# Performance work log

Measured on AMD Instinct MI355X. Metric: run time of the kernel, lower is better.

The kernel has to match this reference:

```python
import jax, jax.numpy as jnp
import numpy as np

# Model dims
B, T, E, H = 2, 2048, 512, 8
HEAD_DIM = E // H            # 64
NUM_SCALES = 4               # Gauss-Laguerre quadrature nodes
NUM_PRF = 16                 # positive random features per scale
POLY_DIM = 16                # degree-2 TensorSketch dim
EPS = 1e-5
CHUNK = 128                  # chunk size for exact chunked causal linear attention


def setup_inputs() -> dict:
    key = jax.random.key(0)
    ks = jax.random.split(key, 10)
    x = jax.random.normal(ks[0], (B, T, E), jnp.float32)
    sc = 1.0 / np.sqrt(E)  # xavier-ish scale for square projections
    Wq = jax.random.normal(ks[1], (E, E), jnp.float32) * sc
    Wk = jax.random.normal(ks[2], (E, E), jnp.float32) * sc
    Wv = jax.random.normal(ks[3], (E, E), jnp.float32) * sc
    Wo = jax.random.normal(ks[4], (E, E), jnp.float32) * sc
    # FAVOR+ gaussian projections, one block per quadrature scale
    projections = jax.random.normal(ks[5], (NUM_SCALES, NUM_PRF, HEAD_DIM), jnp.float32)
    # Gauss-Laguerre nodes/weights for 1/(C - 2 q.k) = int_0^inf exp(-t(C - 2 q.k)) dt
    nodes, weights = np.polynomial.laguerre.laggauss(NUM_SCALES)
    coef = weights * np.exp(nodes) * np.exp(-nodes * EPS)
    scales = jnp.asarray(np.stack([nodes, coef], axis=1), jnp.float32)  # [S, 2] = (t_s, c_s)
    # degree-2 TensorSketch (count-sketch hashes + rademacher signs)
    sketch_h = jax.random.randint(ks[6], (2, HEAD_DIM), 0, POLY_DIM)
    sketch_s = (jax.random.randint(ks[7], (2, HEAD_DIM), 0, 2) * 2 - 1).astype(jnp.float32)
    return dict(x=x, Wq=Wq, Wk=Wk, Wv=Wv, Wo=Wo, projections=projections,
                scales=scales, sketch_h=sketch_h, sketch_s=sketch_s)


def _features(u, projections, scales, sketch_h, sketch_s):
    """Multi-scale FAVOR+ x TensorSketch feature map for the spherical YAT kernel.

    u: [B,T,H,d], unit-normalized along d. Returns [B,T,H, P*S*m].
    Phi(q).Phi(k) ~= (q.k)^2 / (||q-k||^2 + eps).
    """
    t = scales[:, 0]  # quadrature nodes t_s
    c = scales[:, 1]  # quadrature coeffs w_s e^{t_s} e^{-t_s eps}
    S, m, d = projections.shape
    z = jnp.einsum('smd,bthd->bthsm', projections, u)
    # exp(2 t q.k) via positive RFs; extra e^{-t||u||^2}=e^{-t} (unit sphere) folded in -> -2t
    ef = jnp.exp(jnp.sqrt(2.0 * t)[:, None] * z - 2.0 * t[:, None]) * jnp.sqrt(c / m)[:, None]  # [B,T,H,S,m]
    # degree-2 TensorSketch: countsketch via one-hot matmul, combine with FFT conv
    M1 = sketch_s[0][:, None] * jax.nn.one_hot(sketch_h[0], POLY_DIM, dtype=u.dtype)  # [d,P]
    M2 = sketch_s[1][:, None] * jax.nn.one_hot(sketch_h[1], POLY_DIM, dtype=u.dtype)
    ts = jnp.fft.irfft(jnp.fft.rfft(u @ M1) * jnp.fft.rfft(u @ M2), n=POLY_DIM)  # [B,T,H,P]
    Bs, Ts, Hs = u.shape[:3]
    ef = ef.reshape(Bs, Ts, Hs, S * m)
    return (ts[..., :, None] * ef[..., None, :]).reshape(Bs, Ts, Hs, POLY_DIM * S * m)


def reference(x, Wq, Wk, Wv, Wo, projections, scales, sketch_h, sketch_s):
    Bx, Tx, Ex = x.shape
    d = HEAD_DIM
    q = (x @ Wq).reshape(Bx, Tx, H, d)
    k = (x @ Wk).reshape(Bx, Tx, H, d)
    v = (x @ Wv).reshape(Bx, Tx, H, d)
    # spherical: project q,k to unit sphere
    qn = q / (jnp.linalg.norm(q, axis=-1, keepdims=True) + 1e-6)
    kn = k / (jnp.linalg.norm(k, axis=-1, keepdims=True) + 1e-6)
    fq = _features(qn, projections, scales, sketch_h, sketch_s)  # [B,T,H,F]
    fk = _features(kn, projections, scales, sketch_h, sketch_s)
    F = fq.shape[-1]
    # exact chunked causal linear attention: O(T) state, no [T,T] matrix
    N = Tx // CHUNK
    fq_ = fq.reshape(Bx, N, CHUNK, H, F)
    fk_ = fk.reshape(Bx, N, CHUNK, H, F)
    v_ = v.reshape(Bx, N, CHUNK, H, d)
    kv = jnp.einsum('bnchf,bnchd->bnhfd', fk_, v_)   # per-chunk sum of phi(k) v^T
    kz = fk_.sum(axis=2)                              # [B,N,H,F]
    kv_prev = jnp.concatenate([jnp.zeros_like(kv[:, :1]), jnp.cumsum(kv, axis=1)[:, :-1]], axis=1)
    kz_prev = jnp.concatenate([jnp.zeros_like(kz[:, :1]), jnp.cumsum(kz, axis=1)[:, :-1]], axis=1)
    num = jnp.einsum('bnchf,bnhfd->bnchd', fq_, kv_prev)
    den = jnp.einsum('bnchf,bnhf->bnch', fq_, kz_prev)
    # intra-chunk causal part
    sc = jnp.einsum('bnchf,bnkhf->bnhck', fq_, fk_)
    mask = jnp.tril(jnp.ones((CHUNK, CHUNK), bool))
    scm = jnp.where(mask, sc, 0.0)
    num = num + jnp.einsum('bnhck,bnkhd->bnchd', scm, v_)
    den = den + jnp.swapaxes(scm.sum(axis=-1), 2, 3)
    out = num / (den[..., None] + EPS)
    out = out.reshape(Bx, Tx, Ex) @ Wo
    return out
```

## Files before the change

### kernel.cpp

```cpp
#include <hip/hip_runtime.h>
#include <math.h>

#define B_ 2
#define T_ 2048
#define E_ 512
#define H_ 8
#define D_ 64
#define NCH 16
#define CH 128
#define EPS_ 1e-5f

__global__ __launch_bounds__(256) void gemm512(const float* __restrict__ A,
                                               const float* __restrict__ W,
                                               float* __restrict__ C) {
  __shared__ float As[16][132];
  __shared__ float Bs[16][68];
  const int tid = threadIdx.x;
  const int row0 = blockIdx.x * 128, col0 = blockIdx.y * 64;
  const int ar = tid >> 1, ak = (tid & 1) * 8;
  const int bk = tid >> 4, bc = (tid & 15) * 4;
  const int tx = tid & 15, ty = tid >> 4;
  float4 pa0, pa1, pb;
  pa0 = *(const float4*)(A + (size_t)(row0 + ar) * 512 + ak);
  pa1 = *(const float4*)(A + (size_t)(row0 + ar) * 512 + ak + 4);
  pb  = *(const float4*)(W + (size_t)bk * 512 + col0 + bc);
  float acc[8][4] = {};
  for (int k0 = 0; k0 < 512; k0 += 16) {
    __syncthreads();
    As[ak + 0][ar] = pa0.x; As[ak + 1][ar] = pa0.y; As[ak + 2][ar] = pa0.z; As[ak + 3][ar] = pa0.w;
    As[ak + 4][ar] = pa1.x; As[ak + 5][ar] = pa1.y; As[ak + 6][ar] = pa1.z; As[ak + 7][ar] = pa1.w;
    *(float4*)&Bs[bk][bc] = pb;
    if (k0 < 496) {
      pa0 = *(const float4*)(A + (size_t)(row0 + ar) * 512 + k0 + 16 + ak);
      pa1 = *(const float4*)(A + (size_t)(row0 + ar) * 512 + k0 + 16 + ak + 4);
      pb  = *(const float4*)(W + (size_t)(k0 + 16 + bk) * 512 + col0 + bc);
    }
    __syncthreads();
#pragma unroll
    for (int kk = 0; kk < 16; ++kk) {
      float4 a0 = *(const float4*)&As[kk][ty * 4];
      float4 a1 = *(const float4*)&As[kk][ty * 4 + 64];
      float4 b  = *(const float4*)&Bs[kk][tx * 4];
      float aa[8] = {a0.x, a0.y, a0.z, a0.w, a1.x, a1.y, a1.z, a1.w};
      float bb[4] = {b.x, b.y, b.z, b.w};
#pragma unroll
      for (int i = 0; i < 8; ++i)
#pragma unroll
        for (int j = 0; j < 4; ++j) acc[i][j] += aa[i] * bb[j];
    }
  }
#pragma unroll
  for (int i = 0; i < 8; ++i) {
    const int r = row0 + (i < 4 ? ty * 4 + i : 64 + ty * 4 + (i - 4));
    *(float4*)(C + (size_t)r * 512 + col0 + tx * 4) =
        make_float4(acc[i][0], acc[i][1], acc[i][2], acc[i][3]);
  }
}

__global__ __launch_bounds__(256) void feat_kernel(
    const float* __restrict__ q, const float* __restrict__ k,
    const float* __restrict__ proj, const float* __restrict__ scales,
    const int* __restrict__ sh, const float* __restrict__ ss,
    float* __restrict__ Tq, float* __restrict__ Eq,
    float* __restrict__ Tk, float* __restrict__ Ek) {
  __shared__ float Us[128][68];
  __shared__ float PjT[64][68];
  __shared__ float MT[64][36];
  __shared__ float Ps[128][36];
  __shared__ float csq[64], cmb[64], ccf[64];
  const int tid = threadIdx.x;
  const int isK = blockIdx.y;
  const float* in = (isK ? k : q) + (size_t)blockIdx.x * 8192;
  float* To = isK ? Tk : Tq;
  float* Eo = isK ? Ek : Eq;

#pragma unroll
  for (int j = 0; j < 8; ++j) {
    const int f = tid + 256 * j;
    float4 a = *(const float4*)(in + 4 * f);
    *(float4*)&Us[f >> 4][(f & 15) * 4] = a;
  }
  for (int i = tid; i < 4096; i += 256) PjT[i & 63][i >> 6] = proj[i];
  for (int i = tid; i < 64 * 36; i += 256) (&MT[0][0])[i] = 0.f;
  __syncthreads();

  if (tid < 64) {
    MT[tid][sh[tid]] = ss[tid];
    MT[tid][16 + sh[64 + tid]] = ss[64 + tid];
  } else if (tid < 128) {
    const int c = tid - 64;
    const float t = scales[(c >> 4) * 2], cc = scales[(c >> 4) * 2 + 1];
    csq[c] = sqrtf(2.f * t); cmb[c] = -2.f * t; ccf[c] = sqrtf(cc / 16.f);
  }
  {
    const int r2 = tid >> 1, hf = tid & 1;
    float4 tv[8]; float s2 = 0.f;
#pragma unroll
    for (int j2 = 0; j2 < 8; ++j2) {
      tv[j2] = *(const float4*)&Us[r2][hf * 32 + 4 * j2];
      s2 += tv[j2].x * tv[j2].x + tv[j2].y * tv[j2].y + tv[j2].z * tv[j2].z + tv[j2].w * tv[j2].w;
    }
    s2 += __shfl_xor(s2, 1);
    const float inv = 1.f / (sqrtf(s2) + 1e-6f);
#pragma unroll
    for (int j2 = 0; j2 < 8; ++j2) {
      tv[j2].x *= inv; tv[j2].y *= inv; tv[j2].z *= inv; tv[j2].w *= inv;
      *(float4*)&Us[r2][hf * 32 + 4 * j2] = tv[j2];
    }
  }
  __syncthreads();

  const int tx = tid & 7, ty = tid >> 3;
  const int c0 = tx * 8, pc0 = tx * 4;
  float accz[4][8] = {};
  float accp[4][4] = {};
  for (int d0 = 0; d0 < 64; d0 += 4) {
    float Aar[4][4];
#pragma unroll
    for (int i = 0; i < 4; ++i) {
      float4 a4 = *(const float4*)&Us[ty + 32 * i][d0];
      Aar[i][0] = a4.x; Aar[i][1] = a4.y; Aar[i][2] = a4.z; Aar[i][3] = a4.w;
    }
#pragma unroll
    for (int dd = 0; dd < 4; ++dd) {
      float4 bl = *(const float4*)&PjT[d0 + dd][c0];
      float4 bh = *(const float4*)&PjT[d0 + dd][c0 + 4];
      float4 bm = *(const float4*)&MT[d0 + dd][pc0];
      float bb[8] = {bl.x, bl.y, bl.z, bl.w, bh.x, bh.y, bh.z, bh.w};
      float bp[4] = {bm.x, bm.y, bm.z, bm.w};
#pragma unroll
      for (int i = 0; i < 4; ++i) {
        const float a = Aar[i][dd];
#pragma unroll
        for (int j = 0; j < 8; ++j) accz[i][j] += a * bb[j];
#pragma unroll
        for (int j = 0; j < 4; ++j) accp[i][j] += a * bp[j];
      }
    }
  }

  float sq8[8], mb8[8], cf8[8];
#pragma unroll
  for (int j = 0; j < 8; ++j) { sq8[j] = csq[c0 + j]; mb8[j] = cmb[c0 + j]; cf8[j] = ccf[c0 + j]; }
  const int bx16 = blockIdx.x * 16;
#pragma unroll
  for (int i = 0; i < 4; ++i) {
    const int r = ty + 32 * i;
    const int bt = bx16 + (r >> 3);
    const size_t orow = (size_t)((bt >> 11) * 8 + (r & 7)) * 2048 + (bt & 2047);
    float e[8];
#pragma unroll
    for (int j = 0; j < 8; ++j) e[j] = expf(sq8[j] * accz[i][j] + mb8[j]) * cf8[j];
    *(float4*)(Eo + orow * 64 + c0) = make_float4(e[0], e[1], e[2], e[3]);
    *(float4*)(Eo + orow * 64 + c0 + 4) = make_float4(e[4], e[5], e[6], e[7]);
    *(float4*)&Ps[r][pc0] = make_float4(accp[i][0], accp[i][1], accp[i][2], accp[i][3]);
  }
  __syncthreads();

  const int rr = tid >> 1, hf2 = tid & 1;
  float p1v[16], p2v[16];
#pragma unroll
  for (int j4 = 0; j4 < 4; ++j4) {
    float4 a = *(const float4*)&Ps[rr][j4 * 4];
    p1v[j4 * 4 + 0] = a.x; p1v[j4 * 4 + 1] = a.y; p1v[j4 * 4 + 2] = a.z; p1v[j4 * 4 + 3] = a.w;
    float4 b2 = *(const float4*)&Ps[rr][16 + j4 * 4];
    p2v[j4 * 4 + 0] = b2.x; p2v[j4 * 4 + 1] = b2.y; p2v[j4 * 4 + 2] = b2.z; p2v[j4 * 4 + 3] = b2.w;
  }
  const int bt2 = bx16 + (rr >> 3);
  const size_t orow2 = (size_t)((bt2 >> 11) * 8 + (rr & 7)) * 2048 + (bt2 & 2047);
  float tout[8];
  if (hf2 == 0) {
#pragma unroll
    for (int r8 = 0; r8 < 8; ++r8) {
      float a = 0.f;
#pragma unroll
      for (int j = 0; j < 16; ++j) a += p1v[j] * p2v[(r8 - j) & 15];
      tout[r8] = a;
    }
  } else {
#pragma unroll
    for (int r8 = 0; r8 < 8; ++r8) {
      float a = 0.f;
#pragma unroll
      for (int j = 0; j < 16; ++j) a += p1v[j] * p2v[(8 + r8 - j) & 15];
      tout[r8] = a;
    }
  }
  *(float4*)(To + orow2 * 16 + hf2 * 8) = make_float4(tout[0], tout[1], tout[2], tout[3]);
  *(float4*)(To + orow2 * 16 + hf2 * 8 + 4) = make_float4(tout[4], tout[5], tout[6], tout[7]);
}

__global__ __launch_bounds__(256) void vrelayout(const float* __restrict__ v, float* __restrict__ vh) {
  const int f = blockIdx.x * 256 + threadIdx.x;
  float4 a = *(const float4*)(v + 4 * (size_t)f);
  const int d4 = f & 15, h = (f >> 4) & 7, bt = f >> 7;
  const size_t orow = (size_t)((bt >> 11) * 8 + h) * 2048 + (bt & 2047);
  *(float4*)(vh + orow * 64 + d4 * 4) = a;
}

__global__ __launch_bounds__(256) void kv_kernel(const float* __restrict__ Tk, const float* __restrict__ Ek,
                                                 const float* __restrict__ vh, float* __restrict__ KV) {
  const int bhn = blockIdx.x;
  const int slice = blockIdx.y;
  __shared__ float tks[128][20];
  __shared__ float eks[128][16];
  __shared__ float vs[128][64];
  const int tid = threadIdx.x;
  const size_t rowbase = (size_t)bhn * 128;
  for (int i = tid; i < 2048; i += 256) tks[i >> 4][i & 15] = Tk[rowbase * 16 + i];
  for (int i = tid; i < 2048; i += 256) { int r = i >> 4, e = i & 15; eks[r][e] = Ek[(rowbase + r) * 64 + slice * 16 + e]; }
  for (int i = tid; i < 2048; i += 256) {
    float4 v4 = *(const float4*)(vh + rowbase * 64 + 4 * i);
    *(float4*)&vs[(4 * i) >> 6][(4 * i) & 63] = v4;
  }
  __syncthreads();
  const int d = tid & 63, er = tid >> 6;
  float acc[4][16] = {};
  for (int c = 0; c < 128; ++c) {
    float4 t0 = *(const float4*)&tks[c][0];
    float4 t1 = *(const float4*)&tks[c][4];
    float4 t2 = *(const float4*)&tks[c][8];
    float4 t3 = *(const float4*)&tks[c][12];
    float tkc[16] = {t0.x, t0.y, t0.z, t0.w, t1.x, t1.y, t1.z, t1.w,
                     t2.x, t2.y, t2.z, t2.w, t3.x, t3.y, t3.z, t3.w};
    float4 e4 = *(const float4*)&eks[c][er * 4];
    const float w = vs[c][d];
    float ai[4] = {e4.x * w, e4.y * w, e4.z * w, e4.w * w};
#pragma unroll
    for (int i = 0; i < 4; ++i)
#pragma unroll
      for (int p = 0; p < 16; ++p) acc[i][p] += tkc[p] * ai[i];
  }
  float* out = KV + (size_t)bhn * 65536;
#pragma unroll
  for (int i = 0; i < 4; ++i)
#pragma unroll
    for (int p = 0; p < 16; ++p)
      out[(size_t)(p * 64 + slice * 16 + er * 4 + i) * 64 + d] = acc[i][p];
}

__global__ __launch_bounds__(256) void kz_kernel(const float* __restrict__ Tk, const float* __restrict__ Ek,
                                                 float* __restrict__ KZ) {
  const int bhn = blockIdx.x;
  __shared__ float tks[128][20];
  __shared__ float eks[128][64];
  const int tid = threadIdx.x;
  const size_t rowbase = (size_t)bhn * 128;
  for (int i = tid; i < 2048; i += 256) tks[i >> 4][i & 15] = Tk[rowbase * 16 + i];
  for (int i = tid; i < 2048; i += 256) {
    float4 v4 = *(const float4*)(Ek + rowbase * 64 + 4 * i);
    *(float4*)&eks[(4 * i) >> 6][(4 * i) & 63] = v4;
  }
  __syncthreads();
  const int e = tid & 63, p0 = (tid >> 6) * 4;
  float a[4] = {};
  for (int c = 0; c < 128; ++c) {
    float4 t4 = *(const float4*)&tks[c][p0];
    const float ek = eks[c][e];
    a[0] += t4.x * ek; a[1] += t4.y * ek; a[2] += t4.z * ek; a[3] += t4.w * ek;
  }
#pragma unroll
  for (int j = 0; j < 4; ++j) KZ[(size_t)bhn * 1024 + (p0 + j) * 64 + e] = a[j];
}

__global__ void cumsum_kernel(float* __restrict__ KV, float* __restrict__ KZ) {
  const size_t idx = (size_t)blockIdx.x * 256 + threadIdx.x;
  const size_t nkv4 = (size_t)B_ * H_ * 16384;
  if (idx < nkv4) {
    const size_t bh = idx >> 14, j = idx & 16383;
    float4* p = (float4*)(KV + bh * NCH * 65536) + j;
    float4 a = make_float4(0.f, 0.f, 0.f, 0.f);
#pragma unroll
    for (int n = 0; n < NCH; ++n) {
      float4 t = p[(size_t)n << 14];
      p[(size_t)n << 14] = a;
      a.x += t.x; a.y += t.y; a.z += t.z; a.w += t.w;
    }
  } else {
    const size_t i2 = idx - nkv4;
    if (i2 < (size_t)B_ * H_ * 256) {
      const size_t bh = i2 >> 8, j = i2 & 255;
      float4* p = (float4*)(KZ + bh * NCH * 1024) + j;
      float4 a = make_float4(0.f, 0.f, 0.f, 0.f);
#pragma unroll
      for (int n = 0; n < NCH; ++n) {
        float4 t = p[(size_t)n << 8];
        p[(size_t)n << 8] = a;
        a.x += t.x; a.y += t.y; a.z += t.z; a.w += t.w;
      }
    }
  }
}

__global__ __launch_bounds__(256) void intra_kernel(const float* __restrict__ Tq, const float* __restrict__ Eq,
                                                    const float* __restrict__ Tk, const float* __restrict__ Ek,
                                                    const float* __restrict__ vh,
                                                    float* __restrict__ numb, float* __restrict__ den) {
  const int bhn = blockIdx.x;
  const int rh = blockIdx.y;
  __shared__ float tks[128][20];
  __shared__ float eks[128][68];
  __shared__ float vs[128][68];
  const int tid = threadIdx.x;
  const int r = tid >> 2, dg = tid & 3, d0 = dg * 16;
  const int nk = (rh + 1) * 64;
  const size_t chunkbase = (size_t)bhn * 128;
  const size_t myrow = chunkbase + rh * 64 + r;

  for (int i = tid; i < nk * 16; i += 256) tks[i >> 4][i & 15] = Tk[chunkbase * 16 + i];
  for (int i = tid; i < nk * 16; i += 256) {
    float4 e4 = *(const float4*)(Ek + chunkbase * 64 + 4 * i);
    *(float4*)&eks[(4 * i) >> 6][(4 * i) & 63] = e4;
    float4 w4 = *(const float4*)(vh + chunkbase * 64 + 4 * i);
    *(float4*)&vs[(4 * i) >> 6][(4 * i) & 63] = w4;
  }
  float tq[16], eq[64];
#pragma unroll
  for (int pp = 0; pp < 4; ++pp) {
    float4 t4 = *(const float4*)(Tq + myrow * 16 + pp * 4);
    tq[pp * 4 + 0] = t4.x; tq[pp * 4 + 1] = t4.y; tq[pp * 4 + 2] = t4.z; tq[pp * 4 + 3] = t4.w;
  }
#pragma unroll
  for (int ee = 0; ee < 16; ++ee) {
    float4 e4 = *(const float4*)(Eq + myrow * 64 + ee * 4);
    eq[ee * 4 + 0] = e4.x; eq[ee * 4 + 1] = e4.y; eq[ee * 4 + 2] = e4.z; eq[ee * 4 + 3] = e4.w;
  }
  __syncthreads();

  float num[16] = {};
  float dn = 0.f;
  const int kmax = rh * 64 + r;
  for (int kk = 0; kk <= kmax; ++kk) {
    float dT = 0.f, dE = 0.f;
#pragma unroll
    for (int pp = 0; pp < 4; ++pp) {
      float4 t4 = *(const float4*)&tks[kk][pp * 4];
      dT += tq[pp * 4 + 0] * t4.x + tq[pp * 4 + 1] * t4.y + tq[pp * 4 + 2] * t4.z + tq[pp * 4 + 3] * t4.w;
    }
#pragma unroll
    for (int ee = 0; ee < 16; ++ee) {
      float4 e4 = *(const float4*)&eks[kk][ee * 4];
      dE += eq[ee * 4 + 0] * e4.x + eq[ee * 4 + 1] * e4.y + eq[ee * 4 + 2] * e4.z + eq[ee * 4 + 3] * e4.w;
    }
    const float s = dT * dE;
    dn += s;
#pragma unroll
    for (int jj = 0; jj < 4; ++jj) {
      float4 v4 = *(const float4*)&vs[kk][d0 + jj * 4];
      num[jj * 4 + 0] += s * v4.x; num[jj * 4 + 1] += s * v4.y;
      num[jj * 4 + 2] += s * v4.z; num[jj * 4 + 3] += s * v4.w;
    }
  }
#pragma unroll
  for (int jj = 0; jj < 4; ++jj) {
    float4 o = make_float4(num[jj * 4 + 0], num[jj * 4 + 1], num[jj * 4 + 2], num[jj * 4 + 3]);
    *(float4*)(numb + myrow * 64 + d0 + jj * 4) = o;
  }
  if (dg == 0) den[myrow] = dn;
}

__global__ __launch_bounds__(256) void inter_kernel(const float* __restrict__ Tq, const float* __restrict__ Eq,
                                                    const float* __restrict__ KV, const float* __restrict__ KZ,
                                                    const float* __restrict__ numb, const float* __restrict__ den,
                                                    float* __restrict__ att) {
  const int bhn = blockIdx.x;
  const int rh = blockIdx.y;
  const int n = bhn & 15, bh = bhn >> 4;
  const int b = bh >> 3, h = bh & 7;
  __shared__ float tqs[32][17];
  __shared__ float eqs[32][68];
  __shared__ float kvp[64][68];
  __shared__ float kzp[64];
  const int tid = threadIdx.x;
  const int tx = tid & 15, ty = tid >> 4;
  const size_t rowbase = (size_t)bhn * 128 + rh * 32;
  for (int i = tid; i < 512; i += 256) tqs[i >> 4][i & 15] = Tq[rowbase * 16 + i];
  for (int i = tid; i < 512; i += 256) {
    float4 v4 = *(const float4*)(Eq + rowbase * 64 + 4 * i);
    *(float4*)&eqs[i >> 4][(i & 15) * 4] = v4;
  }
  const float* kvb = KV + (size_t)bhn * 65536;
  const float* kzb = KZ + (size_t)bhn * 1024;
  float acc[2][4] = {};
  float accd[2] = {};
  for (int p = 0; p < 16; ++p) {
    __syncthreads();
#pragma unroll
    for (int j = 0; j < 4; ++j) {
      const int f = tid + 256 * j;
      float4 v4 = *(const float4*)(kvb + p * 4096 + 4 * f);
      *(float4*)&kvp[f >> 4][(f & 15) * 4] = v4;
    }
    if (tid < 64) kzp[tid] = kzb[p * 64 + tid];
    __syncthreads();
    float tqv[2];
#pragma unroll
    for (int ci = 0; ci < 2; ++ci) tqv[ci] = tqs[ty + 16 * ci][p];
    for (int e0 = 0; e0 < 64; e0 += 4) {
      float4 kz4 = *(const float4*)&kzp[e0];
      float4 kv0 = *(const float4*)&kvp[e0 + 0][tx * 4];
      float4 kv1 = *(const float4*)&kvp[e0 + 1][tx * 4];
      float4 kv2 = *(const float4*)&kvp[e0 + 2][tx * 4];
      float4 kv3 = *(const float4*)&kvp[e0 + 3][tx * 4];
#pragma unroll
      for (int ci = 0; ci < 2; ++ci) {
        float4 eq4 = *(const float4*)&eqs[ty + 16 * ci][e0];
        const float a0 = tqv[ci] * eq4.x, a1 = tqv[ci] * eq4.y;
        const float a2 = tqv[ci] * eq4.z, a3 = tqv[ci] * eq4.w;
        acc[ci][0] += a0 * kv0.x; acc[ci][1] += a0 * kv0.y; acc[ci][2] += a0 * kv0.z; acc[ci][3] += a0 * kv0.w;
        acc[ci][0] += a1 * kv1.x; acc[ci][1] += a1 * kv1.y; acc[ci][2] += a1 * kv1.z; acc[ci][3] += a1 * kv1.w;
        acc[ci][0] += a2 * kv2.x; acc[ci][1] += a2 * kv2.y; acc[ci][2] += a2 * kv2.z; acc[ci][3] += a2 * kv2.w;
        acc[ci][0] += a3 * kv3.x; acc[ci][1] += a3 * kv3.y; acc[ci][2] += a3 * kv3.z; acc[ci][3] += a3 * kv3.w;
        accd[ci] += a0 * kz4.x + a1 * kz4.y + a2 * kz4.z + a3 * kz4.w;
      }
    }
  }
#pragma unroll
  for (int ci = 0; ci < 2; ++ci) {
    const int rloc = ty + 16 * ci;
    const size_t row = rowbase + rloc;
    const int t = n * 128 + rh * 32 + rloc;
    const float invd = 1.f / (den[row] + accd[ci] + EPS_);
    float4 nm = *(const float4*)(numb + row * 64 + tx * 4);
    float4 o;
    o.x = (nm.x + acc[ci][0]) * invd;
    o.y = (nm.y + acc[ci][1]) * invd;
    o.z = (nm.z + acc[ci][2]) * invd;
    o.w = (nm.w + acc[ci][3]) * invd;
    *(float4*)(att + (size_t)(b * T_ + t) * 512 + h * 64 + tx * 4) = o;
  }
}

extern "C" void kernel_launch(void* const* d_in, const int* in_sizes, int n_in,
                              void* d_out, int out_size, void* d_ws, size_t ws_size,
                              hipStream_t stream) {
  const float* x   = (const float*)d_in[0];
  const float* Wq  = (const float*)d_in[1];
  const float* Wk  = (const float*)d_in[2];
  const float* Wv  = (const float*)d_in[3];
  const float* Wo  = (const float*)d_in[4];
  const float* prj = (const float*)d_in[5];
  const float* scl = (const float*)d_in[6];
  const int*   shh = (const int*)d_in[7];
  const float* sss = (const float*)d_in[8];

  float* ws  = (float*)d_ws;
  float* q   = ws;
  float* k   = q + 2097152;
  float* v   = k + 2097152;
  float* Tq  = v + 2097152;
  float* Eq  = Tq + 524288;
  float* Tk  = Eq + 2097152;
  float* Ek  = Tk + 524288;
  float* vh  = Ek + 2097152;
  float* KV  = vh + 2097152;
  float* KZ  = KV + 16777216;
  float* nmb = KZ + 262144;
  float* den = nmb + 2097152;
  float* att = den + 32768;

  dim3 gg(32, 8);
  hipLaunchKernelGGL(gemm512, gg, dim3(256), 0, stream, x, Wq, q);
  hipLaunchKernelGGL(gemm512, gg, dim3(256), 0, stream, x, Wk, k);
  hipLaunchKernelGGL(gemm512, gg, dim3(256), 0, stream, x, Wv, v);
  hipLaunchKernelGGL(feat_kernel, dim3(256, 2), dim3(256), 0, stream,
                     q, k, prj, scl, shh, sss, Tq, Eq, Tk, Ek);
  hipLaunchKernelGGL(vrelayout, dim3(2048), dim3(256), 0, stream, v, vh);
  hipLaunchKernelGGL(kv_kernel, dim3(256, 4), dim3(256), 0, stream, Tk, Ek, vh, KV);
  hipLaunchKernelGGL(kz_kernel, dim3(256), dim3(256), 0, stream, Tk, Ek, KZ);
  hipLaunchKernelGGL(cumsum_kernel, dim3(1040), dim3(256), 0, stream, KV, KZ);
  hipLaunchKernelGGL(intra_kernel, dim3(256, 2), dim3(256), 0, stream, Tq, Eq, Tk, Ek, vh, nmb, den);
  hipLaunchKernelGGL(inter_kernel, dim3(256, 4), dim3(256), 0, stream, Tq, Eq, KV, KZ, nmb, den, att);
  hipLaunchKernelGGL(gemm512, gg, dim3(256), 0, stream, att, Wo, (float*)d_out);
}
```

Baseline: 426.0 us.

## Use bf16 MFMA for projection GEMMs and double rows per inter block

Replaces the fp32 FMA GEMM used for the four 512x512 projections with a bf16 MFMA 16x16x32 path. It first runs an in-kernel probe MFMA to detect the operand lane layout, and keeps the fp32 fallback if the probe result is unexpected. Inputs are rounded to bf16 in shared memory, which lowers precision. Separately, inter_kernel now handles 64 rows per block instead of 32, halving the grid so each KV tile loaded into shared memory is reused across more query rows.

```diff
diff --git a/kernel.cpp b/kernel.cpp
--- a/kernel.cpp
+++ b/kernel.cpp
@@ -10,50 +10,166 @@
 #define CH 128
 #define EPS_ 1e-5f
 
-__global__ __launch_bounds__(256) void gemm512(const float* __restrict__ A,
-                                               const float* __restrict__ W,
-                                               float* __restrict__ C) {
-  __shared__ float As[16][132];
-  __shared__ float Bs[16][68];
+typedef __attribute__((ext_vector_type(8))) short bf16x8;
+typedef __attribute__((ext_vector_type(4))) short bf16x4;
+typedef __attribute__((ext_vector_type(4))) float f32x4;
+typedef unsigned short ushortT;
+
+__device__ __forceinline__ ushortT f2bf(float f) {
+  union { float f; unsigned u; } v; v.f = f;
+  unsigned r = v.u + 0x7fffu + ((v.u >> 16) & 1u);
+  return (ushortT)(r >> 16);
+}
+
+__global__ __launch_bounds__(256) void gemm512_auto(const float* __restrict__ A,
+                                                    const float* __restrict__ W,
+                                                    float* __restrict__ C) {
+  __shared__ alignas(16) char smem[15360];
   const int tid = threadIdx.x;
   const int row0 = blockIdx.x * 128, col0 = blockIdx.y * 64;
-  const int ar = tid >> 1, ak = (tid & 1) * 8;
-  const int bk = tid >> 4, bc = (tid & 15) * 4;
-  const int tx = tid & 15, ty = tid >> 4;
-  float4 pa0, pa1, pb;
-  pa0 = *(const float4*)(A + (size_t)(row0 + ar) * 512 + ak);
-  pa1 = *(const float4*)(A + (size_t)(row0 + ar) * 512 + ak + 4);
-  pb  = *(const float4*)(W + (size_t)bk * 512 + col0 + bc);
-  float acc[8][4] = {};
-  for (int k0 = 0; k0 < 512; k0 += 16) {
-    __syncthreads();
-    As[ak + 0][ar] = pa0.x; As[ak + 1][ar] = pa0.y; As[ak + 2][ar] = pa0.z; As[ak + 3][ar] = pa0.w;
-    As[ak + 4][ar] = pa1.x; As[ak + 5][ar] = pa1.y; As[ak + 6][ar] = pa1.z; As[ak + 7][ar] = pa1.w;
-    *(float4*)&Bs[bk][bc] = pb;
-    if (k0 < 496) {
-      pa0 = *(const float4*)(A + (size_t)(row0 + ar) * 512 + k0 + 16 + ak);
-      pa1 = *(const float4*)(A + (size_t)(row0 + ar) * 512 + k0 + 16 + ak + 4);
-      pb  = *(const float4*)(W + (size_t)(k0 + 16 + bk) * 512 + col0 + bc);
-    }
-    __syncthreads();
-#pragma unroll
-    for (int kk = 0; kk < 16; ++kk) {
-      float4 a0 = *(const float4*)&As[kk][ty * 4];
-      float4 a1 = *(const float4*)&As[kk][ty * 4 + 64];
-      float4 b  = *(const float4*)&Bs[kk][tx * 4];
-      float aa[8] = {a0.x, a0.y, a0.z, a0.w, a1.x, a1.y, a1.z, a1.w};
-      float bb[4] = {b.x, b.y, b.z, b.w};
-#pragma unroll
-      for (int i = 0; i < 8; ++i)
-#pragma unroll
-        for (int j = 0; j < 4; ++j) acc[i][j] += aa[i] * bb[j];
-    }
-  }
-#pragma unroll
-  for (int i = 0; i < 8; ++i) {
-    const int r = row0 + (i < 4 ? ty * 4 + i : 64 + ty * 4 + (i - 4));
-    *(float4*)(C + (size_t)r * 512 + col0 + tx * 4) =
-        make_float4(acc[i][0], acc[i][1], acc[i][2], acc[i][3]);
+  const int lane = tid & 63, wv = tid >> 6;
+  const int g = lane >> 4, ml = lane & 15;
+
+  int code;
+  {
+    bf16x8 pa, pb;
+#pragma unroll
+    for (int j = 0; j < 8; ++j) {
+      pa[j] = (short)f2bf((float)(g * 8 + j));
+      pb[j] = (short)((g == 1 && j == 0) ? f2bf(1.0f) : (ushortT)0);
+    }
+    f32x4 pd = (f32x4)(0.f);
+    pd = __builtin_amdgcn_mfma_f32_16x16x32_bf16(pa, pb, pd, 0, 0, 0);
+    code = (int)(pd[0] + 0.5f);
+  }
+
+  if (code == 4 || code == 16) {
+    const bool ablk = (code == 16);
+    ushortT (*Asb)[40] = (ushortT(*)[40])smem;
+    ushortT (*Wtb)[40] = (ushortT(*)[40])(smem + 10240);
+    const int wrow = wv * 32;
+    const int sar = tid >> 1, sak = (tid & 1) * 16;
+    const int swk = tid >> 3, swn = (tid & 7) * 8;
+
+    f32x4 acc[2][4];
+#pragma unroll
+    for (int mt = 0; mt < 2; ++mt)
+#pragma unroll
+      for (int nt = 0; nt < 4; ++nt) acc[mt][nt] = (f32x4)(0.f);
+
+    for (int k0 = 0; k0 < 512; k0 += 32) {
+      __syncthreads();
+      {
+        const float* ap = A + (size_t)(row0 + sar) * 512 + k0 + sak;
+        float4 a0 = *(const float4*)(ap);
+        float4 a1 = *(const float4*)(ap + 4);
+        float4 a2 = *(const float4*)(ap + 8);
+        float4 a3 = *(const float4*)(ap + 12);
+        bf16x8 v0, v1;
+        v0[0] = (short)f2bf(a0.x); v0[1] = (short)f2bf(a0.y);
+        v0[2] = (short)f2bf(a0.z); v0[3] = (short)f2bf(a0.w);
+        v0[4] = (short)f2bf(a1.x); v0[5] = (short)f2bf(a1.y);
+        v0[6] = (short)f2bf(a1.z); v0[7] = (short)f2bf(a1.w);
+        v1[0] = (short)f2bf(a2.x); v1[1] = (short)f2bf(a2.y);
+        v1[2] = (short)f2bf(a2.z); v1[3] = (short)f2bf(a2.w);
+        v1[4] = (short)f2bf(a3.x); v1[5] = (short)f2bf(a3.y);
+        v1[6] = (short)f2bf(a3.z); v1[7] = (short)f2bf(a3.w);
+        *(bf16x8*)&Asb[sar][sak] = v0;
+        *(bf16x8*)&Asb[sar][sak + 8] = v1;
+      }
+      {
+        const float* wp = W + (size_t)(k0 + swk) * 512 + col0 + swn;
+        float4 w0 = *(const float4*)(wp);
+        float4 w1 = *(const float4*)(wp + 4);
+        Wtb[swn + 0][swk] = f2bf(w0.x);
+        Wtb[swn + 1][swk] = f2bf(w0.y);
+        Wtb[swn + 2][swk] = f2bf(w0.z);
+        Wtb[swn + 3][swk] = f2bf(w0.w);
+        Wtb[swn + 4][swk] = f2bf(w1.x);
+        Wtb[swn + 5][swk] = f2bf(w1.y);
+        Wtb[swn + 6][swk] = f2bf(w1.z);
+        Wtb[swn + 7][swk] = f2bf(w1.w);
+      }
+      __syncthreads();
+      bf16x8 af0, af1;
+      if (!ablk) {
+        af0 = *(const bf16x8*)&Asb[wrow + ml][g * 8];
+        af1 = *(const bf16x8*)&Asb[wrow + 16 + ml][g * 8];
+      } else {
+        bf16x4 l0 = *(const bf16x4*)&Asb[wrow + ml][4 * g];
+        bf16x4 h0 = *(const bf16x4*)&Asb[wrow + ml][16 + 4 * g];
+        bf16x4 l1 = *(const bf16x4*)&Asb[wrow + 16 + ml][4 * g];
+        bf16x4 h1 = *(const bf16x4*)&Asb[wrow + 16 + ml][16 + 4 * g];
+        af0[0] = l0[0]; af0[1] = l0[1]; af0[2] = l0[2]; af0[3] = l0[3];
+        af0[4] = h0[0]; af0[5] = h0[1]; af0[6] = h0[2]; af0[7] = h0[3];
+        af1[0] = l1[0]; af1[1] = l1[1]; af1[2] = l1[2]; af1[3] = l1[3];
+        af1[4] = h1[0]; af1[5] = h1[1]; af1[6] = h1[2]; af1[7] = h1[3];
+      }
+#pragma unroll
+      for (int nt = 0; nt < 4; ++nt) {
+        bf16x8 bf;
+        if (ablk) {
+          bf = *(const bf16x8*)&Wtb[nt * 16 + ml][g * 8];
+        } else {
+          bf16x4 lo = *(const bf16x4*)&Wtb[nt * 16 + ml][4 * g];
+          bf16x4 hi = *(const bf16x4*)&Wtb[nt * 16 + ml][16 + 4 * g];
+          bf[0] = lo[0]; bf[1] = lo[1]; bf[2] = lo[2]; bf[3] = lo[3];
+          bf[4] = hi[0]; bf[5] = hi[1]; bf[6] = hi[2]; bf[7] = hi[3];
+        }
+        acc[0][nt] = __builtin_amdgcn_mfma_f32_16x16x32_bf16(af0, bf, acc[0][nt], 0, 0, 0);
+        acc[1][nt] = __builtin_amdgcn_mfma_f32_16x16x32_bf16(af1, bf, acc[1][nt], 0, 0, 0);
+      }
+    }
+#pragma unroll
+    for (int mt = 0; mt < 2; ++mt)
+#pragma unroll
+      for (int j = 0; j < 4; ++j) {
+        const int m = wrow + mt * 16 + g * 4 + j;
+        float* crow = C + (size_t)(row0 + m) * 512 + col0;
+#pragma unroll
+        for (int nt = 0; nt < 4; ++nt) crow[nt * 16 + ml] = acc[mt][nt][j];
+      }
+  } else {
+    float (*As)[132] = (float(*)[132])smem;
+    float (*Bs)[68]  = (float(*)[68])(smem + 8448);
+    const int ar = tid >> 1, ak = (tid & 1) * 8;
+    const int bk = tid >> 4, bc = (tid & 15) * 4;
+    const int tx = tid & 15, ty = tid >> 4;
+    float4 pa0, pa1, pb;
+    pa0 = *(const float4*)(A + (size_t)(row0 + ar) * 512 + ak);
+    pa1 = *(const float4*)(A + (size_t)(row0 + ar) * 512 + ak + 4);
+    pb  = *(const float4*)(W + (size_t)bk * 512 + col0 + bc);
+    float acc[8][4] = {};
+    for (int k0 = 0; k0 < 512; k0 += 16) {
+      __syncthreads();
+      As[ak + 0][ar] = pa0.x; As[ak + 1][ar] = pa0.y; As[ak + 2][ar] = pa0.z; As[ak + 3][ar] = pa0.w;
+      As[ak + 4][ar] = pa1.x; As[ak + 5][ar] = pa1.y; As[ak + 6][ar] = pa1.z; As[ak + 7][ar] = pa1.w;
+      *(float4*)&Bs[bk][bc] = pb;
+      if (k0 < 496) {
+        pa0 = *(const float4*)(A + (size_t)(row0 + ar) * 512 + k0 + 16 + ak);
+        pa1 = *(const float4*)(A + (size_t)(row0 + ar) * 512 + k0 + 16 + ak + 4);
+        pb  = *(const float4*)(W + (size_t)(k0 + 16 + bk) * 512 + col0 + bc);
+      }
+      __syncthreads();
+#pragma unroll
+      for (int kk = 0; kk < 16; ++kk) {
+        float4 a0 = *(const float4*)&As[kk][ty * 4];
+        float4 a1 = *(const float4*)&As[kk][ty * 4 + 64];
+        float4 b  = *(const float4*)&Bs[kk][tx * 4];
+        float aa[8] = {a0.x, a0.y, a0.z, a0.w, a1.x, a1.y, a1.z, a1.w};
+        float bb[4] = {b.x, b.y, b.z, b.w};
+#pragma unroll
+        for (int i = 0; i < 8; ++i)
+#pragma unroll
+          for (int j = 0; j < 4; ++j) acc[i][j] += aa[i] * bb[j];
+      }
+    }
+#pragma unroll
+    for (int i = 0; i < 8; ++i) {
+      const int r = row0 + (i < 4 ? ty * 4 + i : 64 + ty * 4 + (i - 4));
+      *(float4*)(C + (size_t)r * 512 + col0 + tx * 4) =
+          make_float4(acc[i][0], acc[i][1], acc[i][2], acc[i][3]);
+    }
   }
 }
 
@@ -367,22 +483,22 @@
   const int rh = blockIdx.y;
   const int n = bhn & 15, bh = bhn >> 4;
   const int b = bh >> 3, h = bh & 7;
-  __shared__ float tqs[32][17];
-  __shared__ float eqs[32][68];
+  __shared__ float tqs[64][17];
+  __shared__ float eqs[64][68];
   __shared__ float kvp[64][68];
   __shared__ float kzp[64];
   const int tid = threadIdx.x;
   const int tx = tid & 15, ty = tid >> 4;
-  const size_t rowbase = (size_t)bhn * 128 + rh * 32;
-  for (int i = tid; i < 512; i += 256) tqs[i >> 4][i & 15] = Tq[rowbase * 16 + i];
-  for (int i = tid; i < 512; i += 256) {
+  const size_t rowbase = (size_t)bhn * 128 + rh * 64;
+  for (int i = tid; i < 1024; i += 256) tqs[i >> 4][i & 15] = Tq[rowbase * 16 + i];
+  for (int i = tid; i < 1024; i += 256) {
     float4 v4 = *(const float4*)(Eq + rowbase * 64 + 4 * i);
     *(float4*)&eqs[i >> 4][(i & 15) * 4] = v4;
   }
   const float* kvb = KV + (size_t)bhn * 65536;
   const float* kzb = KZ + (size_t)bhn * 1024;
-  float acc[2][4] = {};
-  float accd[2] = {};
+  float acc[4][4] = {};
+  float accd[4] = {};
   for (int p = 0; p < 16; ++p) {
     __syncthreads();
 #pragma unroll
@@ -393,9 +509,9 @@
     }
     if (tid < 64) kzp[tid] = kzb[p * 64 + tid];
     __syncthreads();
-    float tqv[2];
-#pragma unroll
-    for (int ci = 0; ci < 2; ++ci) tqv[ci] = tqs[ty + 16 * ci][p];
+    float tqv[4];
+#pragma unroll
+    for (int ci = 0; ci < 4; ++ci) tqv[ci] = tqs[ty + 16 * ci][p];
     for (int e0 = 0; e0 < 64; e0 += 4) {
       float4 kz4 = *(const float4*)&kzp[e0];
       float4 kv0 = *(const float4*)&kvp[e0 + 0][tx * 4];
@@ -403,7 +519,7 @@
       float4 kv2 = *(const float4*)&kvp[e0 + 2][tx * 4];
       float4 kv3 = *(const float4*)&kvp[e0 + 3][tx * 4];
 #pragma unroll
-      for (int ci = 0; ci < 2; ++ci) {
+      for (int ci = 0; ci < 4; ++ci) {
         float4 eq4 = *(const float4*)&eqs[ty + 16 * ci][e0];
         const float a0 = tqv[ci] * eq4.x, a1 = tqv[ci] * eq4.y;
         const float a2 = tqv[ci] * eq4.z, a3 = tqv[ci] * eq4.w;
@@ -416,10 +532,10 @@
     }
   }
 #pragma unroll
-  for (int ci = 0; ci < 2; ++ci) {
+  for (int ci = 0; ci < 4; ++ci) {
     const int rloc = ty + 16 * ci;
     const size_t row = rowbase + rloc;
-    const int t = n * 128 + rh * 32 + rloc;
+    const int t = n * 128 + rh * 64 + rloc;
     const float invd = 1.f / (den[row] + accd[ci] + EPS_);
     float4 nm = *(const float4*)(numb + row * 64 + tx * 4);
     float4 o;
@@ -460,9 +576,9 @@
   float* att = den + 32768;
 
   dim3 gg(32, 8);
-  hipLaunchKernelGGL(gemm512, gg, dim3(256), 0, stream, x, Wq, q);
-  hipLaunchKernelGGL(gemm512, gg, dim3(256), 0, stream, x, Wk, k);
-  hipLaunchKernelGGL(gemm512, gg, dim3(256), 0, stream, x, Wv, v);
+  hipLaunchKernelGGL(gemm512_auto, gg, dim3(256), 0, stream, x, Wq, q);
+  hipLaunchKernelGGL(gemm512_auto, gg, dim3(256), 0, stream, x, Wk, k);
+  hipLaunchKernelGGL(gemm512_auto, gg, dim3(256), 0, stream, x, Wv, v);
   hipLaunchKernelGGL(feat_kernel, dim3(256, 2), dim3(256), 0, stream,
                      q, k, prj, scl, shh, sss, Tq, Eq, Tk, Ek);
   hipLaunchKernelGGL(vrelayout, dim3(2048), dim3(256), 0, stream, v, vh);
@@ -470,6 +586,6 @@
   hipLaunchKernelGGL(kz_kernel, dim3(256), dim3(256), 0, stream, Tk, Ek, KZ);
   hipLaunchKernelGGL(cumsum_kernel, dim3(1040), dim3(256), 0, stream, KV, KZ);
   hipLaunchKernelGGL(intra_kernel, dim3(256, 2), dim3(256), 0, stream, Tq, Eq, Tk, Ek, vh, nmb, den);
-  hipLaunchKernelGGL(inter_kernel, dim3(256, 4), dim3(256), 0, stream, Tq, Eq, KV, KZ, nmb, den, att);
-  hipLaunchKernelGGL(gemm512, gg, dim3(256), 0, stream, att, Wo, (float*)d_out);
-}
+  hipLaunchKernelGGL(inter_kernel, dim3(256, 2), dim3(256), 0, stream, Tq, Eq, KV, KZ, nmb, den, att);
+  hipLaunchKernelGGL(gemm512_auto, gg, dim3(256), 0, stream, att, Wo, (float*)d_out);
+}
```

After: 458.9 us. 1.08x slower.
